# Optimization experiments

Hardware: AMD Instinct MI355X
Metric: run time of the kernel (lower is better)

## Reference

```python
import jax, jax.numpy as jnp
import numpy as np
import math

C = 256
N_HEAD = 8
GROUPS = 32
EPS = 1e-5


def group_norm(x, scale, bias, groups=GROUPS, eps=EPS):
    # x: [B, C, H, W]
    b, c, h, w = x.shape
    xg = x.reshape(b, groups, c // groups, h, w)
    mean = xg.mean(axis=(2, 3, 4), keepdims=True)
    var = xg.var(axis=(2, 3, 4), keepdims=True)
    xg = (xg - mean) * jax.lax.rsqrt(var + eps)
    x = xg.reshape(b, c, h, w)
    return x * scale[None, :, None, None] + bias[None, :, None, None]


def setup_inputs() -> dict:
    key = jax.random.key(0)
    ks = jax.random.split(key, 8)
    B, H, W = 8, 32, 32
    inp = {
        "input_q": jax.random.normal(ks[0], (B, C, H, W), dtype=jnp.float32),
        "input_kv": jax.random.normal(ks[1], (B, C, H, W), dtype=jnp.float32),
        # GroupNorm affine params (torch default: weight=1, bias=0)
        "gq_scale": jnp.ones((C,), jnp.float32),
        "gq_bias": jnp.zeros((C,), jnp.float32),
        "gkv_scale": jnp.ones((C,), jnp.float32),
        "gkv_bias": jnp.zeros((C,), jnp.float32),
        # 1x1 convs as [out, in] matrices
        "Wq": jax.random.normal(ks[2], (C, C), dtype=jnp.float32) / math.sqrt(C),
        "Wkv": jax.random.normal(ks[3], (2 * C, C), dtype=jnp.float32) / math.sqrt(C),
        "Wout": jax.random.normal(ks[4], (C, C), dtype=jnp.float32) / math.sqrt(C),
        "bout": jnp.zeros((C,), jnp.float32),
    }
    return inp


def reference(input_q, input_kv, gq_scale, gq_bias, gkv_scale, gkv_bias, Wq, Wkv, Wout, bout):
    b, c, h, w = input_q.shape
    n = N_HEAD
    d = c // n

    norm_q = group_norm(input_q, gq_scale, gq_bias)
    query = jnp.einsum('oc,bchw->bohw', Wq, norm_q).reshape(b, n, d, h, w)

    norm_kv = group_norm(input_kv, gkv_scale, gkv_bias)
    kv = jnp.einsum('oc,bchw->bohw', Wkv, norm_kv).reshape(b, n, 2 * d, h, w)
    key, value = kv[:, :, :d], kv[:, :, d:]

    attn = jnp.einsum('bnchw,bncyx->bnhwyx', query, key) / math.sqrt(c)
    attn = jax.nn.softmax(attn.reshape(b, n, h, w, h * w), axis=-1)
    attn = attn.reshape(b, n, h, w, h, w)

    out = jnp.einsum('bnhwyx,bncyx->bnchw', attn, value).reshape(b, c, h, w)
    out = jnp.einsum('oc,bchw->bohw', Wout, out) + bout[None, :, None, None]
    return out + input_q
```

## Files before the change

### kernel.cpp

```cpp
#include <hip/hip_runtime.h>
#include <hip/hip_bf16.h>
#include <math.h>
#include <string.h>

#define NB 8
#define NC 256
#define HWSZ 1024
#define NHEAD 8
#define DHEAD 32
#define NGRP 32
#define CPG 8
#define EPSV 1e-5f

typedef float f32x4 __attribute__((ext_vector_type(4)));
typedef short bf16x8 __attribute__((ext_vector_type(8)));

__device__ __forceinline__ unsigned pk2(float a, float b) {
    __hip_bfloat162 h = __float22bfloat162_rn(make_float2(a, b));
    unsigned r;
    memcpy(&r, &h, sizeof(r));
    return r;
}
__device__ __forceinline__ unsigned pk2t(float a, float b) {
    unsigned ua = __float_as_uint(a), ub = __float_as_uint(b);
    return (ua >> 16) | (ub & 0xFFFF0000u);
}
__device__ __forceinline__ unsigned short f2bf(float x) {
    __hip_bfloat16 h = __float2bfloat16(x);
    unsigned short r;
    memcpy(&r, &h, sizeof(r));
    return r;
}
__device__ __forceinline__ float ex2(float x) { return __builtin_amdgcn_exp2f(x); }

__device__ __forceinline__ void gload_lds16(const void* g, void* l) {
    __builtin_amdgcn_global_load_lds(
        (const __attribute__((address_space(1))) unsigned int*)g,
        (__attribute__((address_space(3))) unsigned int*)l, 16, 0, 0);
}

__global__ void prep_kernel(const float* __restrict__ xq,
                            const float* __restrict__ xkv,
                            float* __restrict__ stats,
                            const float* __restrict__ Wq,
                            const float* __restrict__ Wkv,
                            const float* __restrict__ Wout,
                            unsigned short* __restrict__ wqb,
                            unsigned short* __restrict__ wkvb,
                            unsigned short* __restrict__ woutb) {
    if (blockIdx.x < 512) {
        int idx = blockIdx.x;
        int which = idx >> 8;
        int b = (idx >> 5) & 7;
        int g = idx & 31;
        const float* x = which ? xkv : xq;
        const float4* xb = (const float4*)(x + ((size_t)(b * NC + g * CPG)) * HWSZ);
        float s = 0.f, ss = 0.f;
        for (int i = threadIdx.x; i < (CPG * HWSZ) / 4; i += 256) {
            float4 v = xb[i];
            s += v.x + v.y + v.z + v.w;
            ss += v.x * v.x + v.y * v.y + v.z * v.z + v.w * v.w;
        }
        #pragma unroll
        for (int off = 32; off > 0; off >>= 1) {
            s += __shfl_down(s, off);
            ss += __shfl_down(ss, off);
        }
        __shared__ float red[8];
        int wid = threadIdx.x >> 6;
        if ((threadIdx.x & 63) == 0) { red[wid * 2] = s; red[wid * 2 + 1] = ss; }
        __syncthreads();
        if (threadIdx.x == 0) {
            float S = red[0] + red[2] + red[4] + red[6];
            float SS = red[1] + red[3] + red[5] + red[7];
            float mean = S * (1.f / (CPG * HWSZ));
            float var = SS * (1.f / (CPG * HWSZ)) - mean * mean;
            stats[idx * 2] = mean;
            stats[idx * 2 + 1] = rsqrtf(var + EPSV);
        }
    } else {
        int gid = (blockIdx.x - 512) * 256 + threadIdx.x;
        int i0 = gid * 8;
        const float* src; unsigned short* dst; int off; float sc = 1.f;
        if (i0 < 65536)       { src = Wq;   dst = wqb;   off = i0;          sc = 0.0625f * 1.44269504088896f; }
        else if (i0 < 196608) { src = Wkv;  dst = wkvb;  off = i0 - 65536; }
        else                  { src = Wout; dst = woutb; off = i0 - 196608; }
        float4 v0 = *(const float4*)&src[off];
        float4 v1 = *(const float4*)&src[off + 4];
        uint4 o;
        o.x = pk2(v0.x * sc, v0.y * sc); o.y = pk2(v0.z * sc, v0.w * sc);
        o.z = pk2(v1.x * sc, v1.y * sc); o.w = pk2(v1.z * sc, v1.w * sc);
        *(uint4*)&dst[off] = o;
    }
}

__global__ __launch_bounds__(256) void qkv_gemm_kernel(
        const unsigned short* __restrict__ wqb,
        const unsigned short* __restrict__ wkvb,
        const float* __restrict__ xq, const float* __restrict__ xkv,
        const float* __restrict__ stats,
        const float* __restrict__ sq, const float* __restrict__ bq,
        const float* __restrict__ skv, const float* __restrict__ bkv,
        unsigned short* __restrict__ qbuf,
        unsigned short* __restrict__ kbuf,
        unsigned short* __restrict__ vbuf) {
    __shared__ unsigned short As[64 * 256];
    __shared__ unsigned short Bs[64 * 256];
    const int tid = threadIdx.x;
    const int l16 = tid & 15, g = (tid >> 4) & 3, w = tid >> 6;
    const int y = blockIdx.y;
    const bool isQ = y < 4;
    const int o0 = (isQ ? y : y - 4) * 64;
    const size_t prow0 = (size_t)blockIdx.x * 64;
    const int b = (int)(prow0 >> 10);
    const int pp = (int)(prow0 & 1023);

    const unsigned short* Asrc = (isQ ? wqb : wkvb) + (size_t)o0 * NC;
    const float* X  = (isQ ? xq : xkv) + (size_t)b * NC * HWSZ + pp;
    const float* st = stats + (isQ ? 0 : 512) + b * 64;
    const float* sc = isQ ? sq : skv;
    const float* bi = isQ ? bq : bkv;

    #pragma unroll
    for (int it = 0; it < 2; ++it) {
        int idx = tid + it * 256;
        int row = idx >> 3, seg2 = idx & 7;
        #pragma unroll
        for (int q4 = 0; q4 < 4; ++q4) {
            int seg = seg2 * 4 + q4;
            int ds = row * 256 + ((seg ^ (row & 7)) << 3);
            *(uint4*)&As[ds] = *(const uint4*)&Asrc[(size_t)row * NC + seg * 8];
        }
    }
    const int cq = tid >> 4, pq = tid & 15;
    #pragma unroll
    for (int j = 0; j < 4; ++j) {
        int cb = cq * 4 + j * 64;
        int grp = cb >> 3;
        float mean = st[grp * 2], rstd = st[grp * 2 + 1];
        float mm[4][4];
        #pragma unroll
        for (int u = 0; u < 4; ++u) {
            int c = cb + u;
            float4 v = *(const float4*)&X[(size_t)c * HWSZ + pq * 4];
            float a = rstd * sc[c];
            float bbv = bi[c] - mean * a;
            mm[u][0] = v.x * a + bbv; mm[u][1] = v.y * a + bbv;
            mm[u][2] = v.z * a + bbv; mm[u][3] = v.w * a + bbv;
        }
        #pragma unroll
        for (int v2 = 0; v2 < 4; ++v2) {
            int row = pq * 4 + v2;
            int ds = row * 256 + ((((cb >> 3) ^ (row & 7))) << 3) + (cb & 7);
            uint2 s2;
            s2.x = pk2(mm[0][v2], mm[1][v2]);
            s2.y = pk2(mm[2][v2], mm[3][v2]);
            *(uint2*)&Bs[ds] = s2;
        }
    }
    __syncthreads();

    f32x4 acc[4] = {};
    const int abase = (w * 16 + l16) * 256;
    const int asw = l16 & 7;
    #pragma unroll
    for (int kk = 0; kk < 8; ++kk) {
        const int koff = ((kk * 4 + g) ^ asw) << 3;
        bf16x8 a = *(const bf16x8*)&As[abase + koff];
        #pragma unroll
        for (int j = 0; j < 4; ++j) {
            bf16x8 bfr = *(const bf16x8*)&Bs[(j * 16 + l16) * 256 + koff];
            acc[j] = __builtin_amdgcn_mfma_f32_16x16x32_bf16(a, bfr, acc[j], 0, 0, 0);
        }
    }

    if (isQ) {
        int ob_ = o0 + 16 * w + 4 * g;
        int n = ob_ >> 5, d0 = ob_ & 31;
        unsigned short* dst = qbuf + ((size_t)(b * NHEAD + n) * HWSZ) * DHEAD + d0;
        #pragma unroll
        for (int j = 0; j < 4; ++j) {
            int p = pp + 16 * j + l16;
            uint2 st2;
            st2.x = pk2(acc[j][0], acc[j][1]);
            st2.y = pk2(acc[j][2], acc[j][3]);
            *(uint2*)&dst[(size_t)p * DHEAD] = st2;
        }
    } else {
        int n = o0 >> 6;
        int d0 = 16 * (w & 1) + 4 * g;
        if (w < 2) {
            unsigned short* dst = kbuf + ((size_t)(b * NHEAD + n) * HWSZ) * DHEAD + d0;
            #pragma unroll
            for (int j = 0; j < 4; ++j) {
                int p = pp + 16 * j + l16;
                uint2 st2;
                st2.x = pk2(acc[j][0], acc[j][1]);
                st2.y = pk2(acc[j][2], acc[j][3]);
                *(uint2*)&dst[(size_t)p * DHEAD] = st2;
            }
        } else {
            unsigned short* dst = vbuf + ((size_t)(b * NHEAD + n) * DHEAD + d0) * HWSZ;
            #pragma unroll
            for (int j = 0; j < 4; ++j) {
                int slot = ((l16 >> 2) << 3) + ((j & 1) << 2) + (l16 & 3);
                int p = pp + 32 * (j >> 1) + slot;
                #pragma unroll
                for (int r = 0; r < 4; ++r)
                    dst[(size_t)r * HWSZ + p] = f2bf(acc[j][r]);
            }
        }
    }
}

__global__ __launch_bounds__(256) void out_gemm_kernel(
        const unsigned short* __restrict__ Abase,
        const unsigned short* __restrict__ Bbase,
        const float* __restrict__ bias_out,
        const float* __restrict__ resid,
        float* __restrict__ out0) {
    __shared__ unsigned short As[64 * 256];
    __shared__ unsigned short Bs[64 * 256];
    const int tid = threadIdx.x;
    const int l16 = tid & 15, g = (tid >> 4) & 3, w = tid >> 6;
    const int o0 = blockIdx.y * 64;
    const size_t prow0 = (size_t)blockIdx.x * 64;
    const unsigned short* Asrc = Abase + prow0 * NC;
    const unsigned short* Bsrc = Bbase + (size_t)o0 * NC;
    #pragma unroll
    for (int it = 0; it < 8; ++it) {
        int idx = tid + it * 256;
        int row = idx >> 5, seg = idx & 31;
        int ds = row * 256 + ((seg ^ (row & 7)) << 3);
        *(uint4*)&As[ds] = *(const uint4*)&Asrc[(size_t)row * NC + seg * 8];
        *(uint4*)&Bs[ds] = *(const uint4*)&Bsrc[(size_t)row * NC + seg * 8];
    }
    __syncthreads();
    f32x4 acc[4] = {};
    const int abase = (w * 16 + l16) * 256;
    const int asw = l16 & 7;
    #pragma unroll
    for (int kk = 0; kk < 8; ++kk) {
        const int koff = ((kk * 4 + g) ^ asw) << 3;
        bf16x8 a = *(const bf16x8*)&As[abase + koff];
        #pragma unroll
        for (int j = 0; j < 4; ++j) {
            bf16x8 b = *(const bf16x8*)&Bs[(j * 16 + l16) * 256 + koff];
            acc[j] = __builtin_amdgcn_mfma_f32_16x16x32_bf16(a, b, acc[j], 0, 0, 0);
        }
    }
    const int b = (int)(prow0 >> 10);
    const int pp = (int)(prow0 & 1023);
    int p_b = pp + 16 * w + 4 * g;
    #pragma unroll
    for (int j = 0; j < 4; ++j) {
        int o = o0 + 16 * j + l16;
        float bo = bias_out[o];
        size_t off = ((size_t)b * NC + o) * HWSZ + p_b;
        float4 rs = *(const float4*)&resid[off];
        float4 vst = make_float4(acc[j][0] + bo + rs.x, acc[j][1] + bo + rs.y,
                                 acc[j][2] + bo + rs.z, acc[j][3] + bo + rs.w);
        *(float4*)&out0[off] = vst;
    }
}

__global__ __launch_bounds__(256) void attn_mfma_kernel(
        const unsigned short* __restrict__ qb,
        const unsigned short* __restrict__ kb,
        const unsigned short* __restrict__ vb,
        unsigned short* __restrict__ ob) {
    __shared__ unsigned short KV[3][4096];
    const int tid = threadIdx.x;
    const int w = tid >> 6, lane = tid & 63;
    const int l16 = lane & 15, g = lane >> 4;
    const int F = blockIdx.y * 16 + blockIdx.x;
    const int bn = (F & 7) * 8 + (F >> 7);
    const int qblk = (F >> 3) & 15;
    const int qp = qblk * 64 + w * 16 + l16;

    bf16x8 qf = *(const bf16x8*)(qb + ((size_t)bn * HWSZ + qp) * DHEAD + g * 8);

    const int kr = tid >> 2, ks = tid & 3;
    const unsigned short* ksrc = kb + (size_t)bn * HWSZ * DHEAD
                               + (size_t)kr * DHEAD + ((ks ^ (kr & 3)) << 3);
    const int vr = tid >> 3, vs = tid & 7;
    const unsigned short* vsrc = vb + (size_t)bn * DHEAD * HWSZ
                               + (size_t)vr * HWSZ + ((vs ^ (vr & 7)) << 3);
    unsigned short* lk = &KV[0][0] + w * 512;
    unsigned short* lv = &KV[0][2048] + w * 512;

#define STAGE(t) do {                                                        \
        int b3_ = (t) % 3; int ti_ = (t) & 15;                               \
        gload_lds16(ksrc + (size_t)ti_ * 64 * DHEAD, lk + b3_ * 4096);       \
        gload_lds16(vsrc + (size_t)ti_ * 64,         lv + b3_ * 4096);       \
    } while (0)

    f32x4 acc0 = {0.f, 0.f, 0.f, 0.f}, acc1 = {0.f, 0.f, 0.f, 0.f};
    f32x4 accl = {0.f, 0.f, 0.f, 0.f};
    const f32x4 z = {0.f, 0.f, 0.f, 0.f};

    const unsigned on2 = 0x3F803F80u;
    uint4 onev = make_uint4(on2, on2, on2, on2);
    bf16x8 ones;
    memcpy(&ones, &onev, sizeof(ones));

    const int ksw  = (g ^ (l16 & 3)) << 3;
    const int vsw0 = ((g)     ^ (l16 & 7)) << 3;
    const int vsw1 = ((4 + g) ^ (l16 & 7)) << 3;

    STAGE(0);
    STAGE(1);

    #pragma unroll
    for (int t = 0; t < 16; ++t) {
        const int cur = t % 3;
        asm volatile("s_waitcnt vmcnt(2)" ::: "memory");
        __builtin_amdgcn_s_barrier();
        STAGE(t + 2);

        const unsigned short* Kb = &KV[cur][0];
        const unsigned short* Vb = &KV[cur][2048];
        bf16x8 ka0 = *(const bf16x8*)&Kb[(l16)      * 32 + ksw];
        bf16x8 ka1 = *(const bf16x8*)&Kb[(16 + l16) * 32 + ksw];
        bf16x8 ka2 = *(const bf16x8*)&Kb[(32 + l16) * 32 + ksw];
        bf16x8 ka3 = *(const bf16x8*)&Kb[(48 + l16) * 32 + ksw];

        __builtin_amdgcn_s_setprio(1);
        f32x4 s0 = __builtin_amdgcn_mfma_f32_16x16x32_bf16(ka0, qf, z, 0, 0, 0);
        f32x4 s1 = __builtin_amdgcn_mfma_f32_16x16x32_bf16(ka1, qf, z, 0, 0, 0);
        f32x4 s2 = __builtin_amdgcn_mfma_f32_16x16x32_bf16(ka2, qf, z, 0, 0, 0);
        f32x4 s3 = __builtin_amdgcn_mfma_f32_16x16x32_bf16(ka3, qf, z, 0, 0, 0);
        __builtin_amdgcn_s_setprio(0);

        float p00 = ex2(s0[0]), p01 = ex2(s0[1]);
        float p02 = ex2(s0[2]), p03 = ex2(s0[3]);
        float p10 = ex2(s1[0]), p11 = ex2(s1[1]);
        float p12 = ex2(s1[2]), p13 = ex2(s1[3]);
        float p20 = ex2(s2[0]), p21 = ex2(s2[1]);
        float p22 = ex2(s2[2]), p23 = ex2(s2[3]);
        float p30 = ex2(s3[0]), p31 = ex2(s3[1]);
        float p32 = ex2(s3[2]), p33 = ex2(s3[3]);

        uint4 pwa, pwb;
        pwa.x = pk2t(p00, p01); pwa.y = pk2t(p02, p03);
        pwa.z = pk2t(p10, p11); pwa.w = pk2t(p12, p13);
        pwb.x = pk2t(p20, p21); pwb.y = pk2t(p22, p23);
        pwb.z = pk2t(p30, p31); pwb.w = pk2t(p32, p33);
        bf16x8 pf0, pf1;
        memcpy(&pf0, &pwa, sizeof(pf0));
        memcpy(&pf1, &pwb, sizeof(pf1));

        bf16x8 va0 = *(const bf16x8*)&Vb[(l16)      * 64 + vsw0];
        bf16x8 va1 = *(const bf16x8*)&Vb[(l16)      * 64 + vsw1];
        bf16x8 vb0 = *(const bf16x8*)&Vb[(16 + l16) * 64 + vsw0];
        bf16x8 vb1 = *(const bf16x8*)&Vb[(16 + l16) * 64 + vsw1];

        __builtin_amdgcn_s_setprio(1);
        acc0 = __builtin_amdgcn_mfma_f32_16x16x32_bf16(va0, pf0, acc0, 0, 0, 0);
        acc0 = __builtin_amdgcn_mfma_f32_16x16x32_bf16(va1, pf1, acc0, 0, 0, 0);
        acc1 = __builtin_amdgcn_mfma_f32_16x16x32_bf16(vb0, pf0, acc1, 0, 0, 0);
        acc1 = __builtin_amdgcn_mfma_f32_16x16x32_bf16(vb1, pf1, acc1, 0, 0, 0);
        accl = __builtin_amdgcn_mfma_f32_16x16x32_bf16(ones, pf0, accl, 0, 0, 0);
        accl = __builtin_amdgcn_mfma_f32_16x16x32_bf16(ones, pf1, accl, 0, 0, 0);
        __builtin_amdgcn_s_setprio(0);
    }
#undef STAGE

    float invl = 1.f / accl[0];

    const int b = bn >> 3, n = bn & 7;
    unsigned short* dst = ob + ((size_t)b * HWSZ + qp) * NC + n * DHEAD;
    uint2 st0, st1;
    st0.x = pk2(acc0[0] * invl, acc0[1] * invl);
    st0.y = pk2(acc0[2] * invl, acc0[3] * invl);
    st1.x = pk2(acc1[0] * invl, acc1[1] * invl);
    st1.y = pk2(acc1[2] * invl, acc1[3] * invl);
    *(uint2*)&dst[4 * g]      = st0;
    *(uint2*)&dst[16 + 4 * g] = st1;
}

extern "C" void kernel_launch(void* const* d_in, const int* in_sizes, int n_in,
                              void* d_out, int out_size, void* d_ws, size_t ws_size,
                              hipStream_t stream) {
    const float* input_q  = (const float*)d_in[0];
    const float* input_kv = (const float*)d_in[1];
    const float* gq_scale = (const float*)d_in[2];
    const float* gq_bias  = (const float*)d_in[3];
    const float* gkv_scale = (const float*)d_in[4];
    const float* gkv_bias  = (const float*)d_in[5];
    const float* Wq   = (const float*)d_in[6];
    const float* Wkv  = (const float*)d_in[7];
    const float* Wout = (const float*)d_in[8];
    const float* bout = (const float*)d_in[9];
    float* out = (float*)d_out;

    char* ws = (char*)d_ws;
    float* stats = (float*)ws;
    unsigned short* wqb   = (unsigned short*)(ws + 16384);
    unsigned short* wkvb  = (unsigned short*)(ws + 16384 + 131072);
    unsigned short* woutb = (unsigned short*)(ws + 16384 + 131072 + 262144);
    const size_t MB = 1024 * 1024;
    unsigned short* qbuf = (unsigned short*)(ws + 1 * MB);
    unsigned short* kbuf = (unsigned short*)(ws + 5 * MB);
    unsigned short* vbuf = (unsigned short*)(ws + 9 * MB);
    unsigned short* obuf = (unsigned short*)(ws + 13 * MB);

    prep_kernel<<<640, 256, 0, stream>>>(input_q, input_kv, stats,
                                         Wq, Wkv, Wout, wqb, wkvb, woutb);
    qkv_gemm_kernel<<<dim3(128, 12), 256, 0, stream>>>(
        wqb, wkvb, input_q, input_kv, stats,
        gq_scale, gq_bias, gkv_scale, gkv_bias, qbuf, kbuf, vbuf);
    attn_mfma_kernel<<<dim3(16, 64), 256, 0, stream>>>(qbuf, kbuf, vbuf, obuf);
    out_gemm_kernel<<<dim3(128, 4), 256, 0, stream>>>(obuf, woutb, bout, input_q, out);
}
```

Measured before the change: 49.02 us.

## Retile QKV GEMM so each block normalizes 16 pixels once for all outputs

The QKV projection kernel moves from 64x64 output tiles (grid 128x12) to blocks of 16 pixels that compute all 768 output channels (grid 64x8). Each input pixel is now loaded and group-normalized into LDS once instead of once per output tile, which removes repeated reads of the float inputs. Weights are read straight from global memory (L2) as MFMA A fragments rather than staged in LDS. The trade-off is only 512 blocks, more weight traffic per block and less MFMA reuse per B fragment, and the V stores are now scattered at half width.

```diff
diff --git a/kernel.cpp b/kernel.cpp
--- a/kernel.cpp
+++ b/kernel.cpp
@@ -104,38 +104,22 @@
         unsigned short* __restrict__ qbuf,
         unsigned short* __restrict__ kbuf,
         unsigned short* __restrict__ vbuf) {
-    __shared__ unsigned short As[64 * 256];
-    __shared__ unsigned short Bs[64 * 256];
+    __shared__ unsigned short BqS[16 * 256];
+    __shared__ unsigned short BkvS[16 * 256];
     const int tid = threadIdx.x;
     const int l16 = tid & 15, g = (tid >> 4) & 3, w = tid >> 6;
-    const int y = blockIdx.y;
-    const bool isQ = y < 4;
-    const int o0 = (isQ ? y : y - 4) * 64;
-    const size_t prow0 = (size_t)blockIdx.x * 64;
-    const int b = (int)(prow0 >> 10);
-    const int pp = (int)(prow0 & 1023);
-
-    const unsigned short* Asrc = (isQ ? wqb : wkvb) + (size_t)o0 * NC;
-    const float* X  = (isQ ? xq : xkv) + (size_t)b * NC * HWSZ + pp;
-    const float* st = stats + (isQ ? 0 : 512) + b * 64;
-    const float* sc = isQ ? sq : skv;
-    const float* bi = isQ ? bq : bkv;
-
-    #pragma unroll
-    for (int it = 0; it < 2; ++it) {
-        int idx = tid + it * 256;
-        int row = idx >> 3, seg2 = idx & 7;
-        #pragma unroll
-        for (int q4 = 0; q4 < 4; ++q4) {
-            int seg = seg2 * 4 + q4;
-            int ds = row * 256 + ((seg ^ (row & 7)) << 3);
-            *(uint4*)&As[ds] = *(const uint4*)&Asrc[(size_t)row * NC + seg * 8];
-        }
-    }
-    const int cq = tid >> 4, pq = tid & 15;
-    #pragma unroll
-    for (int j = 0; j < 4; ++j) {
-        int cb = cq * 4 + j * 64;
+    const int b = blockIdx.y;
+    const int pp = blockIdx.x * 16;
+
+    const int cq = tid & 63, pq = tid >> 6;
+    const int cb = cq * 4;
+    #pragma unroll
+    for (int which = 0; which < 2; ++which) {
+        const float* X  = (which ? xkv : xq) + (size_t)b * NC * HWSZ + pp;
+        const float* st = stats + which * 512 + b * 64;
+        const float* sc = which ? skv : sq;
+        const float* bi = which ? bkv : bq;
+        unsigned short* Bs = which ? BkvS : BqS;
         int grp = cb >> 3;
         float mean = st[grp * 2], rstd = st[grp * 2 + 1];
         float mm[4][4];
@@ -160,54 +144,49 @@
     }
     __syncthreads();
 
-    f32x4 acc[4] = {};
-    const int abase = (w * 16 + l16) * 256;
     const int asw = l16 & 7;
-    #pragma unroll
-    for (int kk = 0; kk < 8; ++kk) {
-        const int koff = ((kk * 4 + g) ^ asw) << 3;
-        bf16x8 a = *(const bf16x8*)&As[abase + koff];
-        #pragma unroll
-        for (int j = 0; j < 4; ++j) {
-            bf16x8 bfr = *(const bf16x8*)&Bs[(j * 16 + l16) * 256 + koff];
-            acc[j] = __builtin_amdgcn_mfma_f32_16x16x32_bf16(a, bfr, acc[j], 0, 0, 0);
-        }
-    }
-
-    if (isQ) {
+    const int arow = (16 * w + l16) * NC;
+    #pragma unroll
+    for (int y2 = 0; y2 < 12; ++y2) {
+        const bool isQ = y2 < 4;
+        const int o0 = (isQ ? y2 : y2 - 4) * 64;
+        const unsigned short* Asrc = (isQ ? wqb : wkvb) + (size_t)o0 * NC + arow;
+        const unsigned short* Bs = isQ ? BqS : BkvS;
+        f32x4 acc = {0.f, 0.f, 0.f, 0.f};
+        #pragma unroll
+        for (int kk = 0; kk < 8; ++kk) {
+            bf16x8 a = *(const bf16x8*)&Asrc[(kk * 4 + g) << 3];
+            bf16x8 bfr = *(const bf16x8*)&Bs[l16 * 256 + (((kk * 4 + g) ^ asw) << 3)];
+            acc = __builtin_amdgcn_mfma_f32_16x16x32_bf16(a, bfr, acc, 0, 0, 0);
+        }
         int ob_ = o0 + 16 * w + 4 * g;
-        int n = ob_ >> 5, d0 = ob_ & 31;
-        unsigned short* dst = qbuf + ((size_t)(b * NHEAD + n) * HWSZ) * DHEAD + d0;
-        #pragma unroll
-        for (int j = 0; j < 4; ++j) {
-            int p = pp + 16 * j + l16;
+        if (isQ) {
+            int n = ob_ >> 5, d0 = ob_ & 31;
+            int p = pp + l16;
+            unsigned short* dst = qbuf + (((size_t)(b * NHEAD + n) * HWSZ) + p) * DHEAD + d0;
             uint2 st2;
-            st2.x = pk2(acc[j][0], acc[j][1]);
-            st2.y = pk2(acc[j][2], acc[j][3]);
-            *(uint2*)&dst[(size_t)p * DHEAD] = st2;
-        }
-    } else {
-        int n = o0 >> 6;
-        int d0 = 16 * (w & 1) + 4 * g;
-        if (w < 2) {
-            unsigned short* dst = kbuf + ((size_t)(b * NHEAD + n) * HWSZ) * DHEAD + d0;
-            #pragma unroll
-            for (int j = 0; j < 4; ++j) {
-                int p = pp + 16 * j + l16;
+            st2.x = pk2(acc[0], acc[1]);
+            st2.y = pk2(acc[2], acc[3]);
+            *(uint2*)dst = st2;
+        } else {
+            int n = y2 - 4;
+            int d0 = 16 * (w & 1) + 4 * g;
+            if (w < 2) {
+                int p = pp + l16;
+                unsigned short* dst = kbuf + (((size_t)(b * NHEAD + n) * HWSZ) + p) * DHEAD + d0;
                 uint2 st2;
-                st2.x = pk2(acc[j][0], acc[j][1]);
-                st2.y = pk2(acc[j][2], acc[j][3]);
-                *(uint2*)&dst[(size_t)p * DHEAD] = st2;
-            }
-        } else {
-            unsigned short* dst = vbuf + ((size_t)(b * NHEAD + n) * DHEAD + d0) * HWSZ;
-            #pragma unroll
-            for (int j = 0; j < 4; ++j) {
-                int slot = ((l16 >> 2) << 3) + ((j & 1) << 2) + (l16 & 3);
-                int p = pp + 32 * (j >> 1) + slot;
+                st2.x = pk2(acc[0], acc[1]);
+                st2.y = pk2(acc[2], acc[3]);
+                *(uint2*)dst = st2;
+            } else {
+                int sel = (pp >> 4) & 1;
+                int p32 = pp & ~31;
+                int slot = ((l16 >> 2) << 3) + (sel << 2) + (l16 & 3);
+                int p = p32 + slot;
+                unsigned short* dst = vbuf + ((size_t)(b * NHEAD + n) * DHEAD + d0) * HWSZ;
                 #pragma unroll
                 for (int r = 0; r < 4; ++r)
-                    dst[(size_t)r * HWSZ + p] = f2bf(acc[j][r]);
+                    dst[(size_t)r * HWSZ + p] = f2bf(acc[r]);
             }
         }
     }
@@ -407,7 +386,7 @@
 
     prep_kernel<<<640, 256, 0, stream>>>(input_q, input_kv, stats,
                                          Wq, Wkv, Wout, wqb, wkvb, woutb);
-    qkv_gemm_kernel<<<dim3(128, 12), 256, 0, stream>>>(
+    qkv_gemm_kernel<<<dim3(64, 8), 256, 0, stream>>>(
         wqb, wkvb, input_q, input_kv, stats,
         gq_scale, gq_bias, gkv_scale, gkv_bias, qbuf, kbuf, vbuf);
     attn_mfma_kernel<<<dim3(16, 64), 256, 0, stream>>>(qbuf, kbuf, vbuf, obuf);
```

Result: slower. 61.87 us (+26.2%).
